# Kernel tuning notes

Hardware: AMD Instinct MI355X
Metric: run time of the kernel (lower is better)

## Reference

```python
import jax, jax.numpy as jnp
import numpy as np

NUM_IDS = 8          # label ids 0..7; id 0 is background (skipped)
DD = 2.5


def setup_inputs() -> dict:
    key = jax.random.key(0)
    k1, k2 = jax.random.split(key)
    embedding_space = jax.random.normal(k1, (8, 32, 512, 512), dtype=jnp.float32)
    label = jax.random.randint(k2, (8, 1, 512, 512), 0, NUM_IDS, dtype=jnp.int32)
    return {"embedding_space": embedding_space, "label": label}


def _per_image_loss(e, l):
    # e: [HW, C] float, l: [HW] int
    sums = jax.ops.segment_sum(e, l, num_segments=NUM_IDS)                 # [K, C]
    counts = jax.ops.segment_sum(jnp.ones(e.shape[0], e.dtype), l,
                                 num_segments=NUM_IDS)                     # [K]
    means = sums / counts[:, None]                                         # [K, C]
    # per-pixel distance to its cluster mean
    d = jnp.sqrt(jnp.sum((e - means[l]) ** 2, axis=-1))                    # [HW]
    per_class_mean_dist = jax.ops.segment_sum(d, l, num_segments=NUM_IDS) / counts
    var_loss = jnp.sum(per_class_mean_dist[1:])       # skip background id 0

    m = means[1:]                                      # [K-1, C] foreground cluster means
    n_clusters = NUM_IDS - 1
    diff = m[:, None, :] - m[None, :, :]
    sq = jnp.sum(diff * diff, axis=-1)                 # [K-1, K-1]
    upper = jnp.triu(jnp.ones((n_clusters, n_clusters), bool), k=1)
    dist = jnp.sqrt(jnp.where(upper, sq, 1.0))         # safe sqrt off-pairs
    hinge = jnp.where(upper & (dist < 2.0 * DD), (2.0 * DD - dist) ** 2, 0.0)
    dist_loss = jnp.sum(hinge) / (n_clusters - 1)
    return (var_loss + dist_loss) / n_clusters


def reference(embedding_space, label):
    b, c, h, w = embedding_space.shape
    emb = embedding_space.transpose(0, 2, 3, 1).reshape(b, h * w, c)  # [B, HW, C]
    lab = label.reshape(b, h * w)                                     # [B, HW]
    losses = jax.vmap(_per_image_loss)(emb, lab)                      # [B]
    return jnp.mean(losses).reshape(1)
```

## Files before the change

kernel.cpp:

```cpp
#include <hip/hip_runtime.h>

#define HW 262144
#define NB 8
#define NC 32
#define NK 8

#define WS_SUMS 0
#define WS_CNT  2048
#define WS_MT   2112
#define WS_DS   4160
#define WS_FLOATS 4224

__global__ __launch_bounds__(256) void k_sums(const float* __restrict__ emb,
                                              const int* __restrict__ lab,
                                              float* __restrict__ sums) {
    __shared__ float slots[256 * 9];
    __shared__ float red[256];
    const int t = threadIdx.x;
    const int f = blockIdx.x;
    const int b = f & 7;
    const int o = f >> 3;
    const int chunk = o >> 5;
    const int c = o & 31;

    float* myslot = &slots[t * 9];
#pragma unroll
    for (int i = 0; i < 9; ++i) myslot[i] = 0.f;

    const float* e = emb + ((size_t)(b * NC + c)) * HW;
    const int* lb = lab + (size_t)b * HW;
    const int base = chunk * 16384;

    for (int it = 0; it < 16; ++it) {
        const int p = base + it * 1024 + t * 4;
        const int4 l4 = *reinterpret_cast<const int4*>(lb + p);
        const float4 e4 = *reinterpret_cast<const float4*>(e + p);
        myslot[l4.x] += e4.x;
        myslot[l4.y] += e4.y;
        myslot[l4.z] += e4.z;
        myslot[l4.w] += e4.w;
    }
    __syncthreads();

    {
        const int k = t & 7, r = t >> 3;
        float s = 0.f;
#pragma unroll
        for (int i = 0; i < 8; ++i) s += slots[(r + 32 * i) * 9 + k];
        red[r * 8 + k] = s;
    }
    __syncthreads();
    if (t < 8) {
        float s = 0.f;
#pragma unroll
        for (int r = 0; r < 32; ++r) s += red[r * 8 + t];
        atomicAdd(&sums[(b * NK + t) * NC + c], s);
    }
}

__global__ __launch_bounds__(256) void k_counts(const int* __restrict__ lab,
                                                float* __restrict__ counts) {
    __shared__ float slots[256 * 9];
    __shared__ float red[256];
    const int t = threadIdx.x;
    const int b = blockIdx.x >> 5;
    const int sub = blockIdx.x & 31;

    float* myslot = &slots[t * 9];
#pragma unroll
    for (int i = 0; i < 9; ++i) myslot[i] = 0.f;

    const int* lb = lab + (size_t)b * HW;
    const int base = sub * 8192;
    for (int it = 0; it < 8; ++it) {
        const int p = base + it * 1024 + t * 4;
        const int4 l4 = *reinterpret_cast<const int4*>(lb + p);
        myslot[l4.x] += 1.f;
        myslot[l4.y] += 1.f;
        myslot[l4.z] += 1.f;
        myslot[l4.w] += 1.f;
    }
    __syncthreads();
    {
        const int k = t & 7, r = t >> 3;
        float s = 0.f;
#pragma unroll
        for (int i = 0; i < 8; ++i) s += slots[(r + 32 * i) * 9 + k];
        red[r * 8 + k] = s;
    }
    __syncthreads();
    if (t < 8) {
        float s = 0.f;
#pragma unroll
        for (int r = 0; r < 32; ++r) s += red[r * 8 + t];
        atomicAdd(&counts[b * NK + t], s);
    }
}

__global__ __launch_bounds__(256) void k_means(const float* __restrict__ sums,
                                               const float* __restrict__ counts,
                                               float* __restrict__ meansT) {
    const int idx = blockIdx.x * 256 + threadIdx.x;
    const int b = idx >> 8;
    const int k = (idx >> 5) & 7;
    const int c = idx & 31;
    meansT[b * 256 + c * 8 + k] = sums[idx] / counts[b * NK + k];
}

__global__ __launch_bounds__(256) void k_dist(const float* __restrict__ emb,
                                              const int* __restrict__ lab,
                                              const float* __restrict__ meansT,
                                              float* __restrict__ distsum) {
    __shared__ float mT[256];
    __shared__ float slots[256 * 9];
    __shared__ float red[256];
    const int t = threadIdx.x;
    const int f = blockIdx.x;
    const int b = f & 7;
    const int chunk = f >> 3;

    mT[t] = meansT[b * 256 + t];
    float* myslot = &slots[t * 9];
#pragma unroll
    for (int i = 0; i < 9; ++i) myslot[i] = 0.f;
    __syncthreads();

    const int p = chunk * 1024 + t * 4;
    const int4 l4 = *reinterpret_cast<const int4*>(lab + (size_t)b * HW + p);
    const float* e = emb + (size_t)b * NC * HW + p;

    float a0 = 0.f, a1 = 0.f, a2 = 0.f, a3 = 0.f;
#pragma unroll 4
    for (int c = 0; c < NC; ++c) {
        const float4 e4 = *reinterpret_cast<const float4*>(e + (size_t)c * HW);
        const float* mrow = &mT[c * 8];
        float d0 = e4.x - mrow[l4.x];
        float d1 = e4.y - mrow[l4.y];
        float d2 = e4.z - mrow[l4.z];
        float d3 = e4.w - mrow[l4.w];
        a0 += d0 * d0;
        a1 += d1 * d1;
        a2 += d2 * d2;
        a3 += d3 * d3;
    }
    myslot[l4.x] += sqrtf(a0);
    myslot[l4.y] += sqrtf(a1);
    myslot[l4.z] += sqrtf(a2);
    myslot[l4.w] += sqrtf(a3);
    __syncthreads();

    {
        const int k = t & 7, r = t >> 3;
        float s = 0.f;
#pragma unroll
        for (int i = 0; i < 8; ++i) s += slots[(r + 32 * i) * 9 + k];
        red[r * 8 + k] = s;
    }
    __syncthreads();
    if (t < 8) {
        float s = 0.f;
#pragma unroll
        for (int r = 0; r < 32; ++r) s += red[r * 8 + t];
        atomicAdd(&distsum[b * NK + t], s);
    }
}

__global__ __launch_bounds__(256) void k_final(const float* __restrict__ ws,
                                               float* __restrict__ out) {
    __shared__ float varl[8], distl[8], lossb[8];
    const int t = threadIdx.x;
    if (t < 8) { varl[t] = 0.f; distl[t] = 0.f; }
    __syncthreads();

    if (t < 64) {
        const int b = t >> 3, k = t & 7;
        if (k >= 1) {
            const float v = ws[WS_DS + b * NK + k] / ws[WS_CNT + b * NK + k];
            atomicAdd(&varl[b], v);
        }
    }
    if (t < 168) {
        const int b = t / 21;
        const int pr = t - b * 21;
        int ii = 1, jj = 2, cnt = 0;
        for (int a = 1; a <= 7; ++a)
            for (int bb = a + 1; bb <= 7; ++bb) {
                if (cnt == pr) { ii = a; jj = bb; }
                ++cnt;
            }
        const float* mTb = ws + WS_MT + b * 256;
        float sq = 0.f;
#pragma unroll
        for (int c = 0; c < NC; ++c) {
            const float d = mTb[c * 8 + ii] - mTb[c * 8 + jj];
            sq += d * d;
        }
        const float dist = sqrtf(sq);
        const float gap = 5.0f - dist;
        const float h = (dist < 5.0f) ? gap * gap : 0.f;
        atomicAdd(&distl[b], h);
    }
    __syncthreads();
    if (t < 8) lossb[t] = (varl[t] + distl[t] * (1.0f / 6.0f)) * (1.0f / 7.0f);
    __syncthreads();
    if (t == 0) {
        float s = 0.f;
#pragma unroll
        for (int b = 0; b < 8; ++b) s += lossb[b];
        out[0] = s * 0.125f;
    }
}

extern "C" void kernel_launch(void* const* d_in, const int* in_sizes, int n_in,
                              void* d_out, int out_size, void* d_ws, size_t ws_size,
                              hipStream_t stream) {
    const float* emb = (const float*)d_in[0];
    const int* lab = (const int*)d_in[1];
    float* out = (float*)d_out;
    float* ws = (float*)d_ws;

    hipMemsetAsync(d_ws, 0, WS_FLOATS * sizeof(float), stream);

    k_sums<<<NB * 16 * NC, 256, 0, stream>>>(emb, lab, ws + WS_SUMS);
    k_counts<<<NB * 32, 256, 0, stream>>>(lab, ws + WS_CNT);
    k_means<<<8, 256, 0, stream>>>(ws + WS_SUMS, ws + WS_CNT, ws + WS_MT);
    k_dist<<<NB * 256, 256, 0, stream>>>(emb, lab, ws + WS_MT, ws + WS_DS);
    k_final<<<1, 256, 0, stream>>>(ws, out);
}
```

Measured before the change: 101.1 us.

## Fuse counts into sums pass, replace atomics with partials, drop memset

Label counting is folded into the sums kernel, where the c==0 blocks count labels for their chunk. Global atomics are replaced by per-block partial results written to the workspace and reduced deterministically in k_means and k_final, which removes the memset and one launch. Embedding loads switch to nontemporal loads and the distance loop is unrolled further. This trades a launch, a memset and atomic contention for small extra reduction work in the final kernels, and makes the c==0 blocks do more work than the others.

```diff
diff --git a/kernel.cpp b/kernel.cpp
--- a/kernel.cpp
+++ b/kernel.cpp
@@ -5,15 +5,17 @@
 #define NC 32
 #define NK 8
 
-#define WS_SUMS 0
-#define WS_CNT  2048
-#define WS_MT   2112
-#define WS_DS   4160
-#define WS_FLOATS 4224
-
-__global__ __launch_bounds__(256) void k_sums(const float* __restrict__ emb,
-                                              const int* __restrict__ lab,
-                                              float* __restrict__ sums) {
+#define WS_PSUM 0
+#define WS_PCNT 32768
+#define WS_MT   33792
+#define WS_CNT  35840
+#define WS_PD   35904
+
+typedef float f4 __attribute__((ext_vector_type(4)));
+
+__global__ __launch_bounds__(256) void k_pass1(const float* __restrict__ emb,
+                                               const int* __restrict__ lab,
+                                               float* __restrict__ ws) {
     __shared__ float slots[256 * 9];
     __shared__ float red[256];
     const int t = threadIdx.x;
@@ -34,7 +36,7 @@
     for (int it = 0; it < 16; ++it) {
         const int p = base + it * 1024 + t * 4;
         const int4 l4 = *reinterpret_cast<const int4*>(lb + p);
-        const float4 e4 = *reinterpret_cast<const float4*>(e + p);
+        const f4 e4 = __builtin_nontemporal_load(reinterpret_cast<const f4*>(e + p));
         myslot[l4.x] += e4.x;
         myslot[l4.y] += e4.y;
         myslot[l4.z] += e4.z;
@@ -54,63 +56,59 @@
         float s = 0.f;
 #pragma unroll
         for (int r = 0; r < 32; ++r) s += red[r * 8 + t];
-        atomicAdd(&sums[(b * NK + t) * NC + c], s);
-    }
-}
-
-__global__ __launch_bounds__(256) void k_counts(const int* __restrict__ lab,
-                                                float* __restrict__ counts) {
-    __shared__ float slots[256 * 9];
-    __shared__ float red[256];
-    const int t = threadIdx.x;
-    const int b = blockIdx.x >> 5;
-    const int sub = blockIdx.x & 31;
-
-    float* myslot = &slots[t * 9];
-#pragma unroll
-    for (int i = 0; i < 9; ++i) myslot[i] = 0.f;
-
-    const int* lb = lab + (size_t)b * HW;
-    const int base = sub * 8192;
-    for (int it = 0; it < 8; ++it) {
-        const int p = base + it * 1024 + t * 4;
-        const int4 l4 = *reinterpret_cast<const int4*>(lb + p);
-        myslot[l4.x] += 1.f;
-        myslot[l4.y] += 1.f;
-        myslot[l4.z] += 1.f;
-        myslot[l4.w] += 1.f;
-    }
-    __syncthreads();
-    {
-        const int k = t & 7, r = t >> 3;
-        float s = 0.f;
-#pragma unroll
-        for (int i = 0; i < 8; ++i) s += slots[(r + 32 * i) * 9 + k];
-        red[r * 8 + k] = s;
-    }
-    __syncthreads();
-    if (t < 8) {
-        float s = 0.f;
-#pragma unroll
-        for (int r = 0; r < 32; ++r) s += red[r * 8 + t];
-        atomicAdd(&counts[b * NK + t], s);
-    }
-}
-
-__global__ __launch_bounds__(256) void k_means(const float* __restrict__ sums,
-                                               const float* __restrict__ counts,
-                                               float* __restrict__ meansT) {
-    const int idx = blockIdx.x * 256 + threadIdx.x;
-    const int b = idx >> 8;
-    const int k = (idx >> 5) & 7;
-    const int c = idx & 31;
-    meansT[b * 256 + c * 8 + k] = sums[idx] / counts[b * NK + k];
+        ws[WS_PSUM + ((size_t)f) * 8 + t] = s;
+    }
+
+    if (c == 0) {
+        __syncthreads();
+#pragma unroll
+        for (int i = 0; i < 9; ++i) myslot[i] = 0.f;
+        for (int it = 0; it < 16; ++it) {
+            const int p = base + it * 1024 + t * 4;
+            const int4 l4 = *reinterpret_cast<const int4*>(lb + p);
+            myslot[l4.x] += 1.f;
+            myslot[l4.y] += 1.f;
+            myslot[l4.z] += 1.f;
+            myslot[l4.w] += 1.f;
+        }
+        __syncthreads();
+        {
+            const int k = t & 7, r = t >> 3;
+            float s = 0.f;
+#pragma unroll
+            for (int i = 0; i < 8; ++i) s += slots[(r + 32 * i) * 9 + k];
+            red[r * 8 + k] = s;
+        }
+        __syncthreads();
+        if (t < 8) {
+            float s = 0.f;
+#pragma unroll
+            for (int r = 0; r < 32; ++r) s += red[r * 8 + t];
+            ws[WS_PCNT + (b * 16 + chunk) * 8 + t] = s;
+        }
+    }
+}
+
+__global__ __launch_bounds__(256) void k_means(float* __restrict__ ws) {
+    const int b = blockIdx.x;
+    const int t = threadIdx.x;
+    const int c = t >> 3, k = t & 7;
+
+    float cnt = 0.f;
+#pragma unroll
+    for (int ch = 0; ch < 16; ++ch) cnt += ws[WS_PCNT + (b * 16 + ch) * 8 + k];
+
+    float s = 0.f;
+#pragma unroll
+    for (int ch = 0; ch < 16; ++ch) s += ws[WS_PSUM + ((size_t)(b + 8 * (c + 32 * ch))) * 8 + k];
+
+    ws[WS_MT + b * 256 + c * 8 + k] = s / cnt;
+    if (c == 0) ws[WS_CNT + b * 8 + k] = cnt;
 }
 
 __global__ __launch_bounds__(256) void k_dist(const float* __restrict__ emb,
                                               const int* __restrict__ lab,
-                                              const float* __restrict__ meansT,
-                                              float* __restrict__ distsum) {
+                                              float* __restrict__ ws) {
     __shared__ float mT[256];
     __shared__ float slots[256 * 9];
     __shared__ float red[256];
@@ -119,7 +117,7 @@
     const int b = f & 7;
     const int chunk = f >> 3;
 
-    mT[t] = meansT[b * 256 + t];
+    mT[t] = ws[WS_MT + b * 256 + t];
     float* myslot = &slots[t * 9];
 #pragma unroll
     for (int i = 0; i < 9; ++i) myslot[i] = 0.f;
@@ -130,9 +128,9 @@
     const float* e = emb + (size_t)b * NC * HW + p;
 
     float a0 = 0.f, a1 = 0.f, a2 = 0.f, a3 = 0.f;
-#pragma unroll 4
+#pragma unroll 8
     for (int c = 0; c < NC; ++c) {
-        const float4 e4 = *reinterpret_cast<const float4*>(e + (size_t)c * HW);
+        const f4 e4 = __builtin_nontemporal_load(reinterpret_cast<const f4*>(e + (size_t)c * HW));
         const float* mrow = &mT[c * 8];
         float d0 = e4.x - mrow[l4.x];
         float d1 = e4.y - mrow[l4.y];
@@ -161,24 +159,40 @@
         float s = 0.f;
 #pragma unroll
         for (int r = 0; r < 32; ++r) s += red[r * 8 + t];
-        atomicAdd(&distsum[b * NK + t], s);
+        ws[WS_PD + ((size_t)f) * 8 + t] = s;
     }
 }
 
 __global__ __launch_bounds__(256) void k_final(const float* __restrict__ ws,
                                                float* __restrict__ out) {
-    __shared__ float varl[8], distl[8], lossb[8];
-    const int t = threadIdx.x;
-    if (t < 8) { varl[t] = 0.f; distl[t] = 0.f; }
-    __syncthreads();
-
-    if (t < 64) {
-        const int b = t >> 3, k = t & 7;
-        if (k >= 1) {
-            const float v = ws[WS_DS + b * NK + k] / ws[WS_CNT + b * NK + k];
-            atomicAdd(&varl[b], v);
-        }
-    }
+    __shared__ float partial[256];
+    __shared__ float distsum[64];
+    __shared__ float varl[8];
+    __shared__ float hingeL[8 * 21];
+    __shared__ float distl[8];
+    const int t = threadIdx.x;
+
+    {
+        const int pidx = t >> 2;
+        const int sub = t & 3;
+        float s = 0.f;
+        for (int j = 0; j < 64; ++j)
+            s += ws[WS_PD + (size_t)(j * 4 + sub) * 64 + pidx];
+        partial[t] = s;
+    }
+    __syncthreads();
+    if (t < 64)
+        distsum[t] = partial[t * 4] + partial[t * 4 + 1] + partial[t * 4 + 2] + partial[t * 4 + 3];
+    __syncthreads();
+
+    if (t < 8) {
+        float v = 0.f;
+#pragma unroll
+        for (int k = 1; k < 8; ++k)
+            v += distsum[t * 8 + k] / ws[WS_CNT + t * 8 + k];
+        varl[t] = v;
+    }
+
     if (t < 168) {
         const int b = t / 21;
         const int pr = t - b * 21;
@@ -197,16 +211,21 @@
         }
         const float dist = sqrtf(sq);
         const float gap = 5.0f - dist;
-        const float h = (dist < 5.0f) ? gap * gap : 0.f;
-        atomicAdd(&distl[b], h);
-    }
-    __syncthreads();
-    if (t < 8) lossb[t] = (varl[t] + distl[t] * (1.0f / 6.0f)) * (1.0f / 7.0f);
+        hingeL[t] = (dist < 5.0f) ? gap * gap : 0.f;
+    }
+    __syncthreads();
+    if (t < 8) {
+        float h = 0.f;
+#pragma unroll
+        for (int pr = 0; pr < 21; ++pr) h += hingeL[t * 21 + pr];
+        distl[t] = h;
+    }
     __syncthreads();
     if (t == 0) {
         float s = 0.f;
 #pragma unroll
-        for (int b = 0; b < 8; ++b) s += lossb[b];
+        for (int b = 0; b < 8; ++b)
+            s += (varl[b] + distl[b] * (1.0f / 6.0f)) * (1.0f / 7.0f);
         out[0] = s * 0.125f;
     }
 }
@@ -219,11 +238,8 @@
     float* out = (float*)d_out;
     float* ws = (float*)d_ws;
 
-    hipMemsetAsync(d_ws, 0, WS_FLOATS * sizeof(float), stream);
-
-    k_sums<<<NB * 16 * NC, 256, 0, stream>>>(emb, lab, ws + WS_SUMS);
-    k_counts<<<NB * 32, 256, 0, stream>>>(lab, ws + WS_CNT);
-    k_means<<<8, 256, 0, stream>>>(ws + WS_SUMS, ws + WS_CNT, ws + WS_MT);
-    k_dist<<<NB * 256, 256, 0, stream>>>(emb, lab, ws + WS_MT, ws + WS_DS);
+    k_pass1<<<NB * 16 * NC, 256, 0, stream>>>(emb, lab, ws);
+    k_means<<<NB, 256, 0, stream>>>(ws);
+    k_dist<<<NB * 256, 256, 0, stream>>>(emb, lab, ws);
     k_final<<<1, 256, 0, stream>>>(ws, out);
 }
```

After: 103.5 us. 2.4% more time.
